# Optimization experiments

Measured on AMD Instinct MI355X. Metric: run time of the kernel, lower is better.

Reference implementation:

```python
import jax, jax.numpy as jnp
import numpy as np

B, S, UNITS = 32, 4096, 512

def setup_inputs() -> dict:
    key = jax.random.key(0)
    ks = jax.random.split(key, 5)
    scale = 1.0 / np.sqrt(UNITS)
    return {
        "s_prev": jax.random.normal(ks[0], (B, UNITS), dtype=jnp.float32),
        "hidden_states": jax.random.normal(ks[1], (B, S, UNITS), dtype=jnp.float32),
        "Ww": jax.random.normal(ks[2], (UNITS, UNITS), dtype=jnp.float32) * scale,
        "Wb": jnp.zeros((UNITS,), dtype=jnp.float32),
        "Uw": jax.random.normal(ks[3], (UNITS, UNITS), dtype=jnp.float32) * scale,
        "Ub": jnp.zeros((UNITS,), dtype=jnp.float32),
        "Vw": jax.random.normal(ks[4], (UNITS, 1), dtype=jnp.float32) * scale,
        "Vb": jnp.zeros((1,), dtype=jnp.float32),
    }

def reference(s_prev, hidden_states, Ww, Wb, Uw, Ub, Vw, Vb):
    # W(s_prev): [B, 1, U] so it broadcasts over seq axis
    W_s = (s_prev @ Ww + Wb)[:, None, :]
    # U(hidden_states): [B, S, U]
    U_h = jnp.einsum('bsu,uv->bsv', hidden_states, Uw) + Ub
    score = jnp.tanh(W_s + U_h)                      # [B, S, U]
    logits = jnp.einsum('bsu,uo->bso', score, Vw) + Vb  # [B, S, 1]
    weights = jax.nn.softmax(logits, axis=1)         # softmax over seq axis
    context = jnp.sum(weights * hidden_states, axis=1)  # [B, U]
    return (context, weights)
```

## Files before the change

### kernel.cpp

```cpp
#include <hip/hip_runtime.h>
#include <hip/hip_bf16.h>

#define UNITS 512
#define SEQ   4096
#define BATCH 32

typedef __attribute__((ext_vector_type(8))) __bf16 bf16x8;
typedef __attribute__((ext_vector_type(4))) float  f32x4;

__device__ __forceinline__ int swzB(int l) { return l ^ (((l >> 6) & 7) << 4); }
__device__ __forceinline__ int swzA(int l) { return l ^ (((l >> 7) & 7) << 4); }

__global__ void k_bprep(const float* __restrict__ Uw, __bf16* __restrict__ UwTt) {
    const int c     = blockIdx.x;
    const int half  = blockIdx.y;
    const int kstep = blockIdx.z;
    const int t     = threadIdx.x;
    const int n = half * 256 + t;
    bf16x8 o;
#pragma unroll
    for (int j = 0; j < 8; j++)
        o[j] = (__bf16)Uw[(size_t)(kstep * 32 + c * 8 + j) * UNITS + n];
    const int tile = kstep * 2 + half;
    char* dst = (char*)UwTt + (size_t)tile * 16384 + swzB(t * 64 + c * 16);
    *(bf16x8*)dst = o;
}

__global__ void k_wsrow(const float* __restrict__ s_prev, const float* __restrict__ Ww,
                        const float* __restrict__ Wb, const float* __restrict__ Ub,
                        float* __restrict__ ws_Ws) {
    __shared__ float sp[UNITS];
    int b = blockIdx.x, t = threadIdx.x;
    sp[t] = s_prev[b * UNITS + t];
    sp[t + 256] = s_prev[b * UNITS + t + 256];
    __syncthreads();
    float a0 = Wb[t] + Ub[t];
    float a1 = Wb[t + 256] + Ub[t + 256];
#pragma unroll 8
    for (int u = 0; u < UNITS; u++) {
        float s = sp[u];
        a0 += s * Ww[u * UNITS + t];
        a1 += s * Ww[u * UNITS + t + 256];
    }
    ws_Ws[b * UNITS + t] = a0;
    ws_Ws[b * UNITS + t + 256] = a1;
}

#define BM 128
#define BN 256
#define BK 32
#define NSTEP (UNITS / BK)

__launch_bounds__(512, 4)
__global__ void k_logits(const float* __restrict__ hidden, const __bf16* __restrict__ UwTt,
                         const float* __restrict__ wsu, const float* __restrict__ Vw,
                         float* __restrict__ lpart) {
    __shared__ float  Af[2][BM * BK];
    __shared__ __bf16 Bb[2][BN * BK];
    __shared__ float  lred[BM][4];

    const int t = threadIdx.x;
    const int lane = t & 63, wv = t >> 6;
    const int wm = wv >> 2, wn = wv & 3;
    const int l15 = lane & 15, l4 = lane >> 4;
    const int gx = blockIdx.x;
    const int m0 = blockIdx.y * BM;
    const int b  = m0 >> 12;

    f32x4 acc[4][4];
#pragma unroll
    for (int i = 0; i < 4; i++)
#pragma unroll
        for (int j = 0; j < 4; j++) acc[i][j] = (f32x4){0.f, 0.f, 0.f, 0.f};

    const int aphys0 = wv * 2048 + lane * 16;
    const int alog0  = swzA(aphys0);
    const int arow0  = alog0 >> 7;
    const int acolb  = alog0 & 127;
    const char* asrc0 = (const char*)(hidden + (size_t)(m0 + arow0) * UNITS) + acolb;
    const char* asrc1 = (const char*)(hidden + (size_t)(m0 + arow0 + 8) * UNITS) + acolb;

    int aoffR[4], boffR[4];
#pragma unroll
    for (int f = 0; f < 4; f++) {
        aoffR[f] = swzA((wm * 64 + f * 16 + l15) * 128 + l4 * 32);
        boffR[f] = swzB((wn * 64 + f * 16 + l15) * 64 + l4 * 16);
    }

    auto issue = [&](int buf, int s) {
        char* adst = (char*)(&Af[buf][0]) + wv * 2048;
        __builtin_amdgcn_global_load_lds(
            (const __attribute__((address_space(1))) void*)(asrc0 + s * 128),
            (__attribute__((address_space(3))) void*)adst, 16, 0, 0);
        __builtin_amdgcn_global_load_lds(
            (const __attribute__((address_space(1))) void*)(asrc1 + s * 128),
            (__attribute__((address_space(3))) void*)(adst + 1024), 16, 0, 0);
        const char* bsrc = (const char*)UwTt + (size_t)(s * 2 + gx) * 16384
                         + wv * 2048 + lane * 16;
        char* bdst = (char*)(&Bb[buf][0]) + wv * 2048;
        __builtin_amdgcn_global_load_lds(
            (const __attribute__((address_space(1))) void*)bsrc,
            (__attribute__((address_space(3))) void*)bdst, 16, 0, 0);
        __builtin_amdgcn_global_load_lds(
            (const __attribute__((address_space(1))) void*)(bsrc + 1024),
            (__attribute__((address_space(3))) void*)(bdst + 1024), 16, 0, 0);
    };

    issue(0, 0);
    issue(1, 1);

#pragma unroll
    for (int s = 0; s < NSTEP; ++s) {
        const int cur = s & 1;
        if (s < NSTEP - 1) asm volatile("s_waitcnt vmcnt(4)" ::: "memory");
        else               asm volatile("s_waitcnt vmcnt(0)" ::: "memory");
        __builtin_amdgcn_s_barrier();

        bf16x8 a[4], bq[4];
#pragma unroll
        for (int fi = 0; fi < 4; fi++) {
            f32x4 r0 = *(const f32x4*)((const char*)(&Af[cur][0]) + aoffR[fi]);
            f32x4 r1 = *(const f32x4*)((const char*)(&Af[cur][0]) + (aoffR[fi] ^ 16));
            bf16x8 av;
            av[0] = (__bf16)r0[0]; av[1] = (__bf16)r0[1];
            av[2] = (__bf16)r0[2]; av[3] = (__bf16)r0[3];
            av[4] = (__bf16)r1[0]; av[5] = (__bf16)r1[1];
            av[6] = (__bf16)r1[2]; av[7] = (__bf16)r1[3];
            a[fi] = av;
        }
#pragma unroll
        for (int fj = 0; fj < 4; fj++)
            bq[fj] = *(const bf16x8*)((const char*)(&Bb[cur][0]) + boffR[fj]);

        asm volatile("s_waitcnt lgkmcnt(0)" ::: "memory");
        __builtin_amdgcn_sched_barrier(0);
        __builtin_amdgcn_s_setprio(1);
#pragma unroll
        for (int fi = 0; fi < 4; fi++)
#pragma unroll
            for (int fj = 0; fj < 4; fj++)
                acc[fi][fj] = __builtin_amdgcn_mfma_f32_16x16x32_bf16(a[fi], bq[fj], acc[fi][fj], 0, 0, 0);
        __builtin_amdgcn_s_setprio(0);
        __builtin_amdgcn_s_barrier();
        if (s + 2 < NSTEP) issue(cur, s + 2);
    }

    float wsub[4], vww[4];
#pragma unroll
    for (int fj = 0; fj < 4; fj++) {
        int n = gx * BN + wn * 64 + fj * 16 + l15;
        wsub[fj] = wsu[b * UNITS + n];
        vww[fj]  = Vw[n];
    }
#pragma unroll
    for (int fi = 0; fi < 4; fi++) {
#pragma unroll
        for (int r = 0; r < 4; r++) {
            float p = 0.f;
#pragma unroll
            for (int fj = 0; fj < 4; fj++) {
                float x = acc[fi][fj][r] + wsub[fj];
                float e = __expf(2.f * x);
                p += vww[fj] * (1.f - 2.f / (e + 1.f));
            }
#pragma unroll
            for (int off = 1; off < 16; off <<= 1) p += __shfl_xor(p, off);
            if (l15 == 0) lred[wm * 64 + fi * 16 + l4 * 4 + r][wn] = p;
        }
    }
    __syncthreads();
    if (t < BM) {
        float s = lred[t][0] + lred[t][1] + lred[t][2] + lred[t][3];
        lpart[(size_t)(m0 + t) * 2 + gx] = s;
    }
}

__global__ void k_softmax(const float* __restrict__ lpart, float* __restrict__ wout) {
    __shared__ float ebuf[SEQ];
    __shared__ float red[8];
    int b = blockIdx.x, t = threadIdx.x;
    int lane = t & 63, wv = t >> 6;
    float m = -1e30f;
#pragma unroll
    for (int i = 0; i < 16; i++) {
        int s = t + i * 256;
        size_t idx = ((size_t)b * SEQ + s) * 2;
        float l = lpart[idx] + lpart[idx + 1];
        ebuf[s] = l;
        m = fmaxf(m, l);
    }
#pragma unroll
    for (int off = 32; off >= 1; off >>= 1) m = fmaxf(m, __shfl_xor(m, off));
    if (lane == 0) red[wv] = m;
    __syncthreads();
    m = fmaxf(fmaxf(red[0], red[1]), fmaxf(red[2], red[3]));
    float zs = 0.f;
#pragma unroll
    for (int i = 0; i < 16; i++) {
        int s = t + i * 256;
        float e = __expf(ebuf[s] - m);
        ebuf[s] = e;
        zs += e;
    }
#pragma unroll
    for (int off = 32; off >= 1; off >>= 1) zs += __shfl_xor(zs, off);
    __syncthreads();
    if (lane == 0) red[wv] = zs;
    __syncthreads();
    float inv = 1.f / (red[0] + red[1] + red[2] + red[3]);
#pragma unroll
    for (int i = 0; i < 16; i++) {
        int s = t + i * 256;
        wout[(size_t)b * SEQ + s] = ebuf[s] * inv;
    }
}

__global__ void k_ctxpart(const float* __restrict__ hidden, const float* __restrict__ wout,
                          float* __restrict__ part) {
    int b = blockIdx.y, c = blockIdx.x, t = threadIdx.x;
    const float* w = wout + (size_t)b * SEQ + c * 128;
    const float* h = hidden + ((size_t)b * SEQ + c * 128) * UNITS;
    float2 acc = make_float2(0.f, 0.f);
#pragma unroll 4
    for (int s = 0; s < 128; s++) {
        float ww = w[s];
        float2 v = ((const float2*)(h + (size_t)s * UNITS))[t];
        acc.x += ww * v.x;
        acc.y += ww * v.y;
    }
    ((float2*)(part + ((size_t)(b * 32 + c)) * UNITS))[t] = acc;
}

__global__ void k_ctxreduce(const float* __restrict__ part, float* __restrict__ ctx) {
    int b = blockIdx.x, t = threadIdx.x;
    float s = 0.f;
#pragma unroll
    for (int c = 0; c < 32; c++) s += part[((size_t)(b * 32 + c)) * UNITS + t];
    ctx[(size_t)b * UNITS + t] = s;
}

extern "C" void kernel_launch(void* const* d_in, const int* in_sizes, int n_in,
                              void* d_out, int out_size, void* d_ws, size_t ws_size,
                              hipStream_t stream) {
    const float* s_prev = (const float*)d_in[0];
    const float* hidden = (const float*)d_in[1];
    const float* Ww     = (const float*)d_in[2];
    const float* Wb     = (const float*)d_in[3];
    const float* Uw     = (const float*)d_in[4];
    const float* Ub     = (const float*)d_in[5];
    const float* Vw     = (const float*)d_in[6];

    float* out  = (float*)d_out;
    float* ctx  = out;
    float* wout = out + BATCH * UNITS;

    float* wsf   = (float*)d_ws;
    float* ws_Ws = wsf;
    float* ws_lp = ws_Ws + BATCH * UNITS;
    float* ws_cp = ws_lp + (size_t)BATCH * SEQ * 2;
    __bf16* UwTt = (__bf16*)(ws_cp + (size_t)BATCH * 32 * UNITS);

    k_bprep<<<dim3(4, 2, 16), dim3(256), 0, stream>>>(Uw, UwTt);
    k_wsrow<<<dim3(32), dim3(256), 0, stream>>>(s_prev, Ww, Wb, Ub, ws_Ws);
    k_logits<<<dim3(2, 1024), dim3(512), 0, stream>>>(hidden, UwTt, ws_Ws, Vw, ws_lp);
    k_softmax<<<dim3(32), dim3(256), 0, stream>>>(ws_lp, wout);
    k_ctxpart<<<dim3(32, 32), dim3(256), 0, stream>>>(hidden, wout, ws_cp);
    k_ctxreduce<<<dim3(32), dim3(512), 0, stream>>>(ws_cp, ctx);
}
```

Measured before the change: 211.4 us.

## Enlarge logits GEMM tile to 256x256x64 with register-staged bf16 A conversion

The logits GEMM now uses 256-row by 256-column tiles with a 64-wide K step. The fp32 hidden activations are loaded through registers, converted to bf16 once and written into a swizzled LDS layout, instead of being converted on every fragment read. The B-prep kernel is changed to match the new 64-K tile layout, and the 1D grid is remapped so blocks sharing gx and batch rows run close together. Each K step is split into four MFMA phases, with the next tile's global loads and LDS stores interleaved between them. The cost is lower occupancy (launch bounds 2) and larger register and LDS use.

```diff
diff --git a/kernel.cpp b/kernel.cpp
--- a/kernel.cpp
+++ b/kernel.cpp
@@ -8,21 +8,28 @@
 typedef __attribute__((ext_vector_type(8))) __bf16 bf16x8;
 typedef __attribute__((ext_vector_type(4))) float  f32x4;
 
-__device__ __forceinline__ int swzB(int l) { return l ^ (((l >> 6) & 7) << 4); }
-__device__ __forceinline__ int swzA(int l) { return l ^ (((l >> 7) & 7) << 4); }
+__device__ __forceinline__ int swz128(int l) { return l ^ (((l >> 7) & 7) << 4); }
+
+#define MFMA(A, B, C) __builtin_amdgcn_mfma_f32_16x16x32_bf16(A, B, C, 0, 0, 0)
+#define GLL(SRC, DST) __builtin_amdgcn_global_load_lds( \
+    (const __attribute__((address_space(1))) void*)(SRC), \
+    (__attribute__((address_space(3))) void*)(DST), 16, 0, 0)
+#define PK8(X, Y) ({ bf16x8 _o; \
+    _o[0]=(__bf16)(X).x; _o[1]=(__bf16)(X).y; _o[2]=(__bf16)(X).z; _o[3]=(__bf16)(X).w; \
+    _o[4]=(__bf16)(Y).x; _o[5]=(__bf16)(Y).y; _o[6]=(__bf16)(Y).z; _o[7]=(__bf16)(Y).w; _o; })
 
 __global__ void k_bprep(const float* __restrict__ Uw, __bf16* __restrict__ UwTt) {
-    const int c     = blockIdx.x;
-    const int half  = blockIdx.y;
-    const int kstep = blockIdx.z;
-    const int t     = threadIdx.x;
-    const int n = half * 256 + t;
+    const int c  = blockIdx.x;
+    const int gx = blockIdx.y;
+    const int t  = blockIdx.z;
+    const int nl = threadIdx.x;
+    const int n  = gx * 256 + nl;
+    const int k0 = t * 64 + c * 8;
     bf16x8 o;
 #pragma unroll
     for (int j = 0; j < 8; j++)
-        o[j] = (__bf16)Uw[(size_t)(kstep * 32 + c * 8 + j) * UNITS + n];
-    const int tile = kstep * 2 + half;
-    char* dst = (char*)UwTt + (size_t)tile * 16384 + swzB(t * 64 + c * 16);
+        o[j] = (__bf16)Uw[(size_t)(k0 + j) * UNITS + n];
+    char* dst = (char*)UwTt + (size_t)(t * 2 + gx) * 32768 + swz128(nl * 128 + c * 16);
     *(bf16x8*)dst = o;
 }
 
@@ -46,114 +53,192 @@
     ws_Ws[b * UNITS + t + 256] = a1;
 }
 
-#define BM 128
-#define BN 256
-#define BK 32
-#define NSTEP (UNITS / BK)
-
-__launch_bounds__(512, 4)
+#define NT 8
+
+__launch_bounds__(512, 2)
 __global__ void k_logits(const float* __restrict__ hidden, const __bf16* __restrict__ UwTt,
                          const float* __restrict__ wsu, const float* __restrict__ Vw,
                          float* __restrict__ lpart) {
-    __shared__ float  Af[2][BM * BK];
-    __shared__ __bf16 Bb[2][BN * BK];
-    __shared__ float  lred[BM][4];
-
-    const int t = threadIdx.x;
-    const int lane = t & 63, wv = t >> 6;
+    __shared__ __bf16 Ab[2][256 * 64];
+    __shared__ __bf16 Bb[2][256 * 64];
+    __shared__ float  lred[256][4];
+
+    const int tid  = threadIdx.x;
+    const int lane = tid & 63, wv = tid >> 6;
     const int wm = wv >> 2, wn = wv & 3;
     const int l15 = lane & 15, l4 = lane >> 4;
-    const int gx = blockIdx.x;
-    const int m0 = blockIdx.y * BM;
+
+    const int id = blockIdx.x;
+    const int gx = (id >> 3) & 1;
+    const int y  = ((id >> 4) << 3) | (id & 7);
+    const int m0 = y * 256;
     const int b  = m0 >> 12;
 
-    f32x4 acc[4][4];
-#pragma unroll
-    for (int i = 0; i < 4; i++)
+    const int xorv  = (l15 & 7) << 4;
+    const int koff0 = (l4 * 16) ^ xorv;
+    const int koff1 = (64 + l4 * 16) ^ xorv;
+    const int aBase = wm * 16384 + l15 * 128;
+    const int bBase = wn * 8192  + l15 * 128;
+
+    const int sr = tid >> 1, sh = tid & 1;
+    const float* aPtr = hidden + (size_t)(m0 + sr) * UNITS + sh * 32;
+    const int wXor = (sr & 7) << 4;
+    int wo0 = sr * 128 + (((sh << 6) | 0 ) ^ wXor);
+    int wo1 = sr * 128 + (((sh << 6) | 16) ^ wXor);
+    int wo2 = sr * 128 + (((sh << 6) | 32) ^ wXor);
+    int wo3 = sr * 128 + (((sh << 6) | 48) ^ wXor);
+
+    const char* bglBase = (const char*)UwTt + (size_t)gx * 32768 + wv * 4096 + lane * 16;
+
+    f32x4 acc[8][4];
+#pragma unroll
+    for (int i = 0; i < 8; i++)
 #pragma unroll
         for (int j = 0; j < 4; j++) acc[i][j] = (f32x4){0.f, 0.f, 0.f, 0.f};
 
-    const int aphys0 = wv * 2048 + lane * 16;
-    const int alog0  = swzA(aphys0);
-    const int arow0  = alog0 >> 7;
-    const int acolb  = alog0 & 127;
-    const char* asrc0 = (const char*)(hidden + (size_t)(m0 + arow0) * UNITS) + acolb;
-    const char* asrc1 = (const char*)(hidden + (size_t)(m0 + arow0 + 8) * UNITS) + acolb;
-
-    int aoffR[4], boffR[4];
-#pragma unroll
-    for (int f = 0; f < 4; f++) {
-        aoffR[f] = swzA((wm * 64 + f * 16 + l15) * 128 + l4 * 32);
-        boffR[f] = swzB((wn * 64 + f * 16 + l15) * 64 + l4 * 16);
-    }
-
-    auto issue = [&](int buf, int s) {
-        char* adst = (char*)(&Af[buf][0]) + wv * 2048;
-        __builtin_amdgcn_global_load_lds(
-            (const __attribute__((address_space(1))) void*)(asrc0 + s * 128),
-            (__attribute__((address_space(3))) void*)adst, 16, 0, 0);
-        __builtin_amdgcn_global_load_lds(
-            (const __attribute__((address_space(1))) void*)(asrc1 + s * 128),
-            (__attribute__((address_space(3))) void*)(adst + 1024), 16, 0, 0);
-        const char* bsrc = (const char*)UwTt + (size_t)(s * 2 + gx) * 16384
-                         + wv * 2048 + lane * 16;
-        char* bdst = (char*)(&Bb[buf][0]) + wv * 2048;
-        __builtin_amdgcn_global_load_lds(
-            (const __attribute__((address_space(1))) void*)bsrc,
-            (__attribute__((address_space(3))) void*)bdst, 16, 0, 0);
-        __builtin_amdgcn_global_load_lds(
-            (const __attribute__((address_space(1))) void*)(bsrc + 1024),
-            (__attribute__((address_space(3))) void*)(bdst + 1024), 16, 0, 0);
-    };
-
-    issue(0, 0);
-    issue(1, 1);
-
-#pragma unroll
-    for (int s = 0; s < NSTEP; ++s) {
-        const int cur = s & 1;
-        if (s < NSTEP - 1) asm volatile("s_waitcnt vmcnt(4)" ::: "memory");
-        else               asm volatile("s_waitcnt vmcnt(0)" ::: "memory");
-        __builtin_amdgcn_s_barrier();
-
-        bf16x8 a[4], bq[4];
-#pragma unroll
-        for (int fi = 0; fi < 4; fi++) {
-            f32x4 r0 = *(const f32x4*)((const char*)(&Af[cur][0]) + aoffR[fi]);
-            f32x4 r1 = *(const f32x4*)((const char*)(&Af[cur][0]) + (aoffR[fi] ^ 16));
-            bf16x8 av;
-            av[0] = (__bf16)r0[0]; av[1] = (__bf16)r0[1];
-            av[2] = (__bf16)r0[2]; av[3] = (__bf16)r0[3];
-            av[4] = (__bf16)r1[0]; av[5] = (__bf16)r1[1];
-            av[6] = (__bf16)r1[2]; av[7] = (__bf16)r1[3];
-            a[fi] = av;
-        }
-#pragma unroll
-        for (int fj = 0; fj < 4; fj++)
-            bq[fj] = *(const bf16x8*)((const char*)(&Bb[cur][0]) + boffR[fj]);
-
+    {
+        float4 p0 = *(const float4*)(aPtr + 0);
+        float4 p1 = *(const float4*)(aPtr + 4);
+        float4 p2 = *(const float4*)(aPtr + 8);
+        float4 p3 = *(const float4*)(aPtr + 12);
+        float4 p4 = *(const float4*)(aPtr + 16);
+        float4 p5 = *(const float4*)(aPtr + 20);
+        float4 p6 = *(const float4*)(aPtr + 24);
+        float4 p7 = *(const float4*)(aPtr + 28);
+        GLL(bglBase,        (char*)Bb[0] + wv * 4096);
+        GLL(bglBase + 1024, (char*)Bb[0] + wv * 4096 + 1024);
+        GLL(bglBase + 2048, (char*)Bb[0] + wv * 4096 + 2048);
+        GLL(bglBase + 3072, (char*)Bb[0] + wv * 4096 + 3072);
+        *(bf16x8*)((char*)Ab[0] + wo0) = PK8(p0, p1);
+        *(bf16x8*)((char*)Ab[0] + wo1) = PK8(p2, p3);
+        *(bf16x8*)((char*)Ab[0] + wo2) = PK8(p4, p5);
+        *(bf16x8*)((char*)Ab[0] + wo3) = PK8(p6, p7);
+        asm volatile("s_waitcnt vmcnt(0) lgkmcnt(0)" ::: "memory");
+        __builtin_amdgcn_s_barrier();
+    }
+
+#pragma unroll
+    for (int kt = 0; kt < NT; ++kt) {
+        char* Ac = (char*)Ab[kt & 1];
+        char* Bc = (char*)Bb[kt & 1];
+        char* An = (char*)Ab[(kt & 1) ^ 1];
+        char* Bn = (char*)Bb[(kt & 1) ^ 1];
+        const bool st = (kt < NT - 1);
+        const float* ap = aPtr + (kt + 1) * 64;
+        const char* bs  = bglBase + (size_t)(kt + 1) * 65536;
+
+        bf16x8 bq[4][2];
+        bf16x8 af0k0, af0k1, af1k0, af1k1;
+        float4 la0, la1, la2, la3, la4, la5, la6, la7;
+
+#pragma unroll
+        for (int fj = 0; fj < 4; fj++) {
+            bq[fj][0] = *(const bf16x8*)(Bc + bBase + fj * 2048 + koff0);
+            bq[fj][1] = *(const bf16x8*)(Bc + bBase + fj * 2048 + koff1);
+        }
+        af0k0 = *(const bf16x8*)(Ac + aBase + 0 * 2048 + koff0);
+        af0k1 = *(const bf16x8*)(Ac + aBase + 0 * 2048 + koff1);
+        af1k0 = *(const bf16x8*)(Ac + aBase + 1 * 2048 + koff0);
+        af1k1 = *(const bf16x8*)(Ac + aBase + 1 * 2048 + koff1);
+        if (st) {
+            la0 = *(const float4*)(ap + 0);
+            la1 = *(const float4*)(ap + 4);
+            la2 = *(const float4*)(ap + 8);
+            la3 = *(const float4*)(ap + 12);
+            GLL(bs,        Bn + wv * 4096);
+            GLL(bs + 1024, Bn + wv * 4096 + 1024);
+        }
         asm volatile("s_waitcnt lgkmcnt(0)" ::: "memory");
         __builtin_amdgcn_sched_barrier(0);
         __builtin_amdgcn_s_setprio(1);
 #pragma unroll
-        for (int fi = 0; fi < 4; fi++)
-#pragma unroll
-            for (int fj = 0; fj < 4; fj++)
-                acc[fi][fj] = __builtin_amdgcn_mfma_f32_16x16x32_bf16(a[fi], bq[fj], acc[fi][fj], 0, 0, 0);
+        for (int fj = 0; fj < 4; fj++) {
+            acc[0][fj] = MFMA(af0k0, bq[fj][0], acc[0][fj]);
+            acc[0][fj] = MFMA(af0k1, bq[fj][1], acc[0][fj]);
+            acc[1][fj] = MFMA(af1k0, bq[fj][0], acc[1][fj]);
+            acc[1][fj] = MFMA(af1k1, bq[fj][1], acc[1][fj]);
+        }
         __builtin_amdgcn_s_setprio(0);
         __builtin_amdgcn_s_barrier();
-        if (s + 2 < NSTEP) issue(cur, s + 2);
+
+        af0k0 = *(const bf16x8*)(Ac + aBase + 2 * 2048 + koff0);
+        af0k1 = *(const bf16x8*)(Ac + aBase + 2 * 2048 + koff1);
+        af1k0 = *(const bf16x8*)(Ac + aBase + 3 * 2048 + koff0);
+        af1k1 = *(const bf16x8*)(Ac + aBase + 3 * 2048 + koff1);
+        if (st) {
+            la4 = *(const float4*)(ap + 16);
+            la5 = *(const float4*)(ap + 20);
+            la6 = *(const float4*)(ap + 24);
+            la7 = *(const float4*)(ap + 28);
+            GLL(bs + 2048, Bn + wv * 4096 + 2048);
+            GLL(bs + 3072, Bn + wv * 4096 + 3072);
+            *(bf16x8*)(An + wo0) = PK8(la0, la1);
+            *(bf16x8*)(An + wo1) = PK8(la2, la3);
+        }
+        asm volatile("s_waitcnt lgkmcnt(0)" ::: "memory");
+        __builtin_amdgcn_sched_barrier(0);
+        __builtin_amdgcn_s_setprio(1);
+#pragma unroll
+        for (int fj = 0; fj < 4; fj++) {
+            acc[2][fj] = MFMA(af0k0, bq[fj][0], acc[2][fj]);
+            acc[2][fj] = MFMA(af0k1, bq[fj][1], acc[2][fj]);
+            acc[3][fj] = MFMA(af1k0, bq[fj][0], acc[3][fj]);
+            acc[3][fj] = MFMA(af1k1, bq[fj][1], acc[3][fj]);
+        }
+        __builtin_amdgcn_s_setprio(0);
+        __builtin_amdgcn_s_barrier();
+
+        af0k0 = *(const bf16x8*)(Ac + aBase + 4 * 2048 + koff0);
+        af0k1 = *(const bf16x8*)(Ac + aBase + 4 * 2048 + koff1);
+        af1k0 = *(const bf16x8*)(Ac + aBase + 5 * 2048 + koff0);
+        af1k1 = *(const bf16x8*)(Ac + aBase + 5 * 2048 + koff1);
+        if (st) {
+            *(bf16x8*)(An + wo2) = PK8(la4, la5);
+        }
+        asm volatile("s_waitcnt lgkmcnt(0)" ::: "memory");
+        __builtin_amdgcn_sched_barrier(0);
+        __builtin_amdgcn_s_setprio(1);
+#pragma unroll
+        for (int fj = 0; fj < 4; fj++) {
+            acc[4][fj] = MFMA(af0k0, bq[fj][0], acc[4][fj]);
+            acc[4][fj] = MFMA(af0k1, bq[fj][1], acc[4][fj]);
+            acc[5][fj] = MFMA(af1k0, bq[fj][0], acc[5][fj]);
+            acc[5][fj] = MFMA(af1k1, bq[fj][1], acc[5][fj]);
+        }
+        __builtin_amdgcn_s_setprio(0);
+        __builtin_amdgcn_s_barrier();
+
+        af0k0 = *(const bf16x8*)(Ac + aBase + 6 * 2048 + koff0);
+        af0k1 = *(const bf16x8*)(Ac + aBase + 6 * 2048 + koff1);
+        af1k0 = *(const bf16x8*)(Ac + aBase + 7 * 2048 + koff0);
+        af1k1 = *(const bf16x8*)(Ac + aBase + 7 * 2048 + koff1);
+        if (st) {
+            *(bf16x8*)(An + wo3) = PK8(la6, la7);
+        }
+        asm volatile("s_waitcnt lgkmcnt(0)" ::: "memory");
+        __builtin_amdgcn_sched_barrier(0);
+        __builtin_amdgcn_s_setprio(1);
+#pragma unroll
+        for (int fj = 0; fj < 4; fj++) {
+            acc[6][fj] = MFMA(af0k0, bq[fj][0], acc[6][fj]);
+            acc[6][fj] = MFMA(af0k1, bq[fj][1], acc[6][fj]);
+            acc[7][fj] = MFMA(af1k0, bq[fj][0], acc[7][fj]);
+            acc[7][fj] = MFMA(af1k1, bq[fj][1], acc[7][fj]);
+        }
+        __builtin_amdgcn_s_setprio(0);
+        if (st) asm volatile("s_waitcnt vmcnt(0)" ::: "memory");
+        __builtin_amdgcn_s_barrier();
     }
 
     float wsub[4], vww[4];
 #pragma unroll
     for (int fj = 0; fj < 4; fj++) {
-        int n = gx * BN + wn * 64 + fj * 16 + l15;
+        int n = gx * 256 + wn * 64 + fj * 16 + l15;
         wsub[fj] = wsu[b * UNITS + n];
         vww[fj]  = Vw[n];
     }
 #pragma unroll
-    for (int fi = 0; fi < 4; fi++) {
+    for (int fi = 0; fi < 8; fi++) {
 #pragma unroll
         for (int r = 0; r < 4; r++) {
             float p = 0.f;
@@ -165,13 +250,13 @@
             }
 #pragma unroll
             for (int off = 1; off < 16; off <<= 1) p += __shfl_xor(p, off);
-            if (l15 == 0) lred[wm * 64 + fi * 16 + l4 * 4 + r][wn] = p;
-        }
-    }
-    __syncthreads();
-    if (t < BM) {
-        float s = lred[t][0] + lred[t][1] + lred[t][2] + lred[t][3];
-        lpart[(size_t)(m0 + t) * 2 + gx] = s;
+            if (l15 == 0) lred[wm * 128 + fi * 16 + l4 * 4 + r][wn] = p;
+        }
+    }
+    __syncthreads();
+    if (tid < 256) {
+        float s = lred[tid][0] + lred[tid][1] + lred[tid][2] + lred[tid][3];
+        lpart[(size_t)(m0 + tid) * 2 + gx] = s;
     }
 }
 
@@ -260,9 +345,9 @@
     float* ws_cp = ws_lp + (size_t)BATCH * SEQ * 2;
     __bf16* UwTt = (__bf16*)(ws_cp + (size_t)BATCH * 32 * UNITS);
 
-    k_bprep<<<dim3(4, 2, 16), dim3(256), 0, stream>>>(Uw, UwTt);
+    k_bprep<<<dim3(8, 2, 8), dim3(256), 0, stream>>>(Uw, UwTt);
     k_wsrow<<<dim3(32), dim3(256), 0, stream>>>(s_prev, Ww, Wb, Ub, ws_Ws);
-    k_logits<<<dim3(2, 1024), dim3(512), 0, stream>>>(hidden, UwTt, ws_Ws, Vw, ws_lp);
+    k_logits<<<dim3(1024), dim3(512), 0, stream>>>(hidden, UwTt, ws_Ws, Vw, ws_lp);
     k_softmax<<<dim3(32), dim3(256), 0, stream>>>(ws_lp, wout);
     k_ctxpart<<<dim3(32, 32), dim3(256), 0, stream>>>(hidden, wout, ws_cp);
     k_ctxreduce<<<dim3(32), dim3(512), 0, stream>>>(ws_cp, ctx);
```

Measured after the change: 255.9 us. +21.0%, slower.
